# Kernel tuning notes

Hardware: AMD Instinct MI355X
Metric: run time of the kernel (lower is better)

## Reference

```python
import jax, jax.numpy as jnp
import numpy as np

B, CIN, C, H, W = 2, 64, 128, 64, 1024
H2, W2 = H // 2, W // 2

def _unfold(x, k, pad, stride, dil=1):
    # F.unfold equivalent -> [B, C, k*k, Ho, Wo] with (kh, kw) row-major ordering
    Bx, Cx, Hx, Wx = x.shape
    Ho = (Hx + 2 * pad - dil * (k - 1) - 1) // stride + 1
    Wo = (Wx + 2 * pad - dil * (k - 1) - 1) // stride + 1
    xp = jnp.pad(x, ((0, 0), (0, 0), (pad, pad), (pad, pad)))
    pats = [xp[:, :, i * dil:i * dil + stride * (Ho - 1) + 1:stride,
                  j * dil:j * dil + stride * (Wo - 1) + 1:stride]
            for i in range(k) for j in range(k)]
    return jnp.stack(pats, axis=2)

def _conv(x, w, b, pad, dil=1):
    y = jax.lax.conv_general_dilated(x, w, (1, 1), ((pad, pad), (pad, pad)),
                                     rhs_dilation=(dil, dil),
                                     dimension_numbers=('NCHW', 'OIHW', 'NCHW'))
    return y + b[None, :, None, None]

def _c1x1(x, w, b):
    return jnp.einsum('oi,bi...->bo...', w, x) + b.reshape((1, -1) + (1,) * (x.ndim - 2))

def _bn(x, s, b):
    shp = (1, -1) + (1,) * (x.ndim - 2)
    return x * s.reshape(shp) + b.reshape(shp)

def _forward(x, xyz, c1_w, c1_b, c2_w, c2_b, c3_w, c3_b, c4_w, c4_b, c5_w, c5_b,
             rbn_s, rbn_b, p_w, p_b, pbn_s, pbn_b, lin_w, lin_b,
             w1_w, w1_b, w2_w, w2_b, w3_w, w3_b,
             wbn1_s, wbn1_b, wbn2_s, wbn2_b, wbn3_s, wbn3_b):
    lrelu, relu = jax.nn.leaky_relu, jax.nn.relu
    # get_group_mask geometry (kernel 5, stride 2): relative neighbor coordinates
    gxyz = _unfold(xyz, 5, 2, 2) - xyz[:, :, ::2, ::2][:, :, None]  # [B,3,25,H2,W2]
    # ResBlock trunk (eval-mode BN folded to per-channel scale/shift)
    shortcut = lrelu(_c1x1(x, c1_w, c1_b))
    resA1 = _bn(lrelu(_conv(x, c2_w, c2_b, pad=1)), rbn_s[0], rbn_b[0])
    resA2 = _bn(lrelu(_conv(resA1, c3_w, c3_b, pad=2, dil=2)), rbn_s[1], rbn_b[1])
    resA3 = _bn(lrelu(_conv(resA2, c4_w, c4_b, pad=1, dil=2)), rbn_s[2], rbn_b[2])
    concat = jnp.concatenate([resA1, resA2, resA3], axis=1)
    resA = _bn(lrelu(_c1x1(concat, c5_w, c5_b)), rbn_s[3], rbn_b[3]) + shortcut
    # PConv downsample: pointwise MLP, WeightNet on geometry, unfold + per-pixel matmul
    h = resA
    for i in range(3):
        h = relu(_bn(_c1x1(h, p_w[i], p_b[i]), pbn_s[i], pbn_b[i]))
    wn = relu(_bn(_c1x1(gxyz, w1_w, w1_b), wbn1_s, wbn1_b))
    wn = relu(_bn(_c1x1(wn, w2_w, w2_b), wbn2_s, wbn2_b))
    wn = relu(_bn(_c1x1(wn, w3_w, w3_b), wbn3_s, wbn3_b))          # [B,16,25,H2,W2]
    unf = _unfold(h, 5, 2, 2)                                      # [B,C,25,H2,W2]
    y = jnp.einsum('bckhw,bnkhw->bcnhw', unf, wn).reshape(B, C * 16, H2, W2)
    resB = relu(_bn(_c1x1(y, lin_w, lin_b), pbn_s[3], pbn_b[3]))   # [B,C,H2,W2]
    return resB, resA

def setup_inputs():
    keys = iter(jax.random.split(jax.random.key(0), 48))
    def rn(shape, scale=0.05):
        return jax.random.normal(next(keys), shape, jnp.float32) * scale
    def bn_pair(shape):
        return 1.0 + rn(shape, 0.1), rn(shape, 0.1)
    d = {}
    d['x'] = rn((B, CIN, H, W), 1.0)
    d['xyz'] = rn((B, 3, H, W), 0.1)
    d['c1_w'], d['c1_b'] = rn((C, CIN)), rn((C,))
    d['c2_w'], d['c2_b'] = rn((C, CIN, 3, 3)), rn((C,))
    d['c3_w'], d['c3_b'] = rn((C, C, 3, 3)), rn((C,))
    d['c4_w'], d['c4_b'] = rn((C, C, 2, 2)), rn((C,))
    d['c5_w'], d['c5_b'] = rn((C, 3 * C)), rn((C,))
    d['rbn_s'], d['rbn_b'] = bn_pair((4, C))
    d['p_w'], d['p_b'] = rn((3, C, C)), rn((3, C))
    d['pbn_s'], d['pbn_b'] = bn_pair((4, C))
    d['lin_w'], d['lin_b'] = rn((C, 16 * C), 0.02), rn((C,))
    d['w1_w'], d['w1_b'] = rn((8, 3), 0.5), rn((8,))
    d['w2_w'], d['w2_b'] = rn((8, 8), 0.5), rn((8,))
    d['w3_w'], d['w3_b'] = rn((16, 8), 0.5), rn((16,))
    d['wbn1_s'], d['wbn1_b'] = bn_pair((8,))
    d['wbn2_s'], d['wbn2_b'] = bn_pair((8,))
    d['wbn3_s'], d['wbn3_b'] = bn_pair((16,))
    return d

def reference(x, xyz, c1_w, c1_b, c2_w, c2_b, c3_w, c3_b, c4_w, c4_b, c5_w, c5_b,
              rbn_s, rbn_b, p_w, p_b, pbn_s, pbn_b, lin_w, lin_b,
              w1_w, w1_b, w2_w, w2_b, w3_w, w3_b,
              wbn1_s, wbn1_b, wbn2_s, wbn2_b, wbn3_s, wbn3_b):
    return _forward(x, xyz, c1_w, c1_b, c2_w, c2_b, c3_w, c3_b, c4_w, c4_b, c5_w, c5_b,
                    rbn_s, rbn_b, p_w, p_b, pbn_s, pbn_b, lin_w, lin_b,
                    w1_w, w1_b, w2_w, w2_b, w3_w, w3_b,
                    wbn1_s, wbn1_b, wbn2_s, wbn2_b, wbn3_s, wbn3_b)
```

## Files before the change

### kernel.cpp

```cpp
#include <hip/hip_runtime.h>
#include <hip/hip_bf16.h>

typedef __hip_bfloat16 bf16;
typedef unsigned short u16;
typedef unsigned int   u32;

#define B_   2
#define CIN_ 64
#define C_   128
#define H_   64
#define W_   1024
#define HW_  (H_*W_)
#define H2_  32
#define W2_  512
#define HW2_ (H2_*W2_)

typedef __attribute__((ext_vector_type(8))) short bf16x8;
typedef __attribute__((ext_vector_type(4))) float f32x4;

#define OFF_C2  0
#define OFF_C3  73728
#define OFF_C4  221184
#define OFF_C5  286720
#define OFF_C1  335872
#define OFF_PW  344064
#define OFF_LIN 393216
#define WTS_TOT 655360
__device__ __align__(16) u16 g_wts[WTS_TOT];
__device__ __align__(16) u16 g_b1[(size_t)B_*C_*HW_];
__device__ __align__(16) u16 g_b2[(size_t)B_*C_*HW_];
__device__ __align__(16) u16 g_b3[(size_t)B_*C_*HW_];
__device__ __align__(16) u16 g_xb[(size_t)B_*HW_*CIN_];

__device__ __forceinline__ float bits2f(u16 u){
    u32 x = ((u32)u) << 16; float f; __builtin_memcpy(&f, &x, 4); return f;
}
__device__ __forceinline__ u16 f2bits(float v){
    bf16 h = __float2bfloat16(v); u16 u; __builtin_memcpy(&u, &h, 2); return u;
}
__device__ __forceinline__ float lrelu(float v){ return v > 0.f ? v : 0.01f*v; }
__device__ __forceinline__ float relu (float v){ return v > 0.f ? v : 0.f; }

#define LSTR 40
#define PSTR 136
#define TSTR 136

__device__ __forceinline__ void stage_A(u16* As, const u16* w, int wstr, int col0, int tid)
{
#pragma unroll
    for (int r = 0; r < 2; r++) {
        int e = tid + 256*r;
        int co = e >> 2, ch = e & 3;
        *(uint4*)&As[co*LSTR + ch*8] = *(const uint4*)&w[co*wstr + col0 + ch*8];
    }
}

__device__ __forceinline__ void stage_B_pm(u16* Bs, const u16* src, int rowStride,
                                           int kc, int tid)
{
#pragma unroll
    for (int r = 0; r < 2; r++) {
        int e = tid + 256*r;
        int j = e >> 2, g = e & 3;
        *(uint4*)&Bs[j*LSTR + g*8] =
            *(const uint4*)&src[(size_t)j*rowStride + kc*32 + g*8];
    }
}

__device__ __forceinline__ void mfma_step_s(const u16* As, const u16* Bs, int bstr, int koff,
                                            int lane, int wm, int wn_, f32x4 acc[4][4])
{
    const int quad = lane >> 4, l15 = lane & 15;
    bf16x8 a[4], b[4];
#pragma unroll
    for (int i = 0; i < 4; i++)
        a[i] = *(const bf16x8*)&As[(wm*64 + i*16 + l15)*LSTR + quad*8];
#pragma unroll
    for (int j = 0; j < 4; j++)
        b[j] = *(const bf16x8*)&Bs[(wn_*64 + j*16 + l15)*bstr + koff + quad*8];
#pragma unroll
    for (int i = 0; i < 4; i++)
#pragma unroll
        for (int j = 0; j < 4; j++)
            acc[i][j] = __builtin_amdgcn_mfma_f32_16x16x32_bf16(a[i], b[j], acc[i][j], 0, 0, 0);
}

__device__ __forceinline__ void mfma_step(const u16* As, const u16* Bs,
                                          int lane, int wm, int wn_, f32x4 acc[4][4])
{
    mfma_step_s(As, Bs, LSTR, 0, lane, wm, wn_, acc);
}

__device__ __forceinline__ void init_bias(f32x4 acc[4][4], const float* bias, int wm, int lane)
{
    const int quad = lane >> 4;
#pragma unroll
    for (int i = 0; i < 4; i++)
#pragma unroll
        for (int r = 0; r < 4; r++) {
            float bv = bias[wm*64 + i*16 + quad*4 + r];
#pragma unroll
            for (int j = 0; j < 4; j++) acc[i][j][r] = bv;
        }
}

#define XTS 70
__global__ __launch_bounds__(256)
void k_xtrans(const float* __restrict__ x0, u16* __restrict__ xb0)
{
    __shared__ __align__(16) u16 T[128*XTS];
    const int tid = threadIdx.x;
    const float* x = x0 + (size_t)blockIdx.y*CIN_*HW_;
    u16* xb = xb0 + (size_t)blockIdx.y*HW_*CIN_;
    const int pix0 = blockIdx.x * 128;
#pragma unroll
    for (int r = 0; r < 8; r++) {
        int e = tid + 256*r;
        int c = e >> 5, p4 = (e & 31)*4;
        float4 v = *(const float4*)&x[(size_t)c*HW_ + pix0 + p4];
        T[(p4+0)*XTS + c] = f2bits(v.x);
        T[(p4+1)*XTS + c] = f2bits(v.y);
        T[(p4+2)*XTS + c] = f2bits(v.z);
        T[(p4+3)*XTS + c] = f2bits(v.w);
    }
    __syncthreads();
#pragma unroll
    for (int r = 0; r < 4; r++) {
        int e = tid + 256*r;
        int p = e >> 3, g = e & 7;
        const u16* s = &T[p*XTS + g*8];
        u16* d = &xb[(size_t)(pix0+p)*CIN_ + g*8];
        *(uint2*)&d[0] = *(const uint2*)&s[0];
        *(uint2*)&d[4] = *(const uint2*)&s[4];
    }
}

template<int CI, int KS, int DIL, int PAD>
__global__ __launch_bounds__(256)
void k_conv(const u16* __restrict__ in0, const u16* __restrict__ wT,
            const float* __restrict__ bias, const float* __restrict__ bns,
            const float* __restrict__ bnb, u16* __restrict__ out0)
{
    __shared__ __align__(16) u16 S[128*TSTR];
    u16* As = S;
    u16* Bs = S + 128*LSTR;
    const int tid = threadIdx.x, lane = tid & 63, wave = tid >> 6;
    const int wm = wave & 1, wn_ = wave >> 1;
    const u16* in = in0 + (size_t)blockIdx.y*HW_*CI;
    u16* out = out0 + (size_t)blockIdx.y*HW_*C_;
    const int pix0 = blockIdx.x * 128;
    const int y = pix0 >> 10, x0 = pix0 & 1023;

    f32x4 acc[4][4];
    init_bias(acc, bias, wm, lane);

    for (int p = 0; p < KS*KS; p++) {
        int dy = (p/KS)*DIL - PAD, dx = (p%KS)*DIL - PAD;
        int yy = y + dy;
        if (yy < 0 || yy >= H_) continue;
        const u16* srow = in + (size_t)yy*W_*CI;
        for (int kc = 0; kc < CI/32; kc++) {
            stage_A(As, wT + p*128*CI, CI, kc*32, tid);
#pragma unroll
            for (int r = 0; r < 2; r++) {
                int e = tid + 256*r;
                int j = e >> 2, g = e & 3;
                int xx = x0 + dx + j;
                uint4 v = make_uint4(0u, 0u, 0u, 0u);
                if ((unsigned)xx < (unsigned)W_)
                    v = *(const uint4*)&srow[(size_t)xx*CI + kc*32 + g*8];
                *(uint4*)&Bs[j*LSTR + g*8] = v;
            }
            __syncthreads();
            mfma_step(As, Bs, lane, wm, wn_, acc);
            __syncthreads();
        }
    }
    const int quad = lane >> 4, l15 = lane & 15;
    u16* T = S;
#pragma unroll
    for (int i = 0; i < 4; i++)
#pragma unroll
        for (int r = 0; r < 4; r++) {
            int co = wm*64 + i*16 + quad*4 + r;
            float ss = bns[co], tt = bnb[co];
#pragma unroll
            for (int j = 0; j < 4; j++) {
                float v = lrelu(acc[i][j][r]) * ss + tt;
                T[(wn_*64 + j*16 + l15)*TSTR + co] = f2bits(v);
            }
        }
    __syncthreads();
#pragma unroll
    for (int r = 0; r < 8; r++) {
        int e = tid + 256*r;
        int px = e >> 4, g = e & 15;
        *(uint4*)&out[(size_t)(pix0+px)*C_ + g*8] = *(const uint4*)&T[px*TSTR + g*8];
    }
}

__global__ __launch_bounds__(256)
void k_resA(const u16* __restrict__ xb0, const u16* __restrict__ a10,
            const u16* __restrict__ a20, const u16* __restrict__ a30,
            const u16* __restrict__ wc1, const float* __restrict__ c1b,
            const u16* __restrict__ wc5, const float* __restrict__ c5b,
            const float* __restrict__ s3, const float* __restrict__ b3,
            float* __restrict__ out0)
{
    __shared__ __align__(16) u16 As[128*LSTR];
    __shared__ __align__(16) u16 Bs[128*LSTR];
    const int tid = threadIdx.x, lane = tid & 63, wave = tid >> 6;
    const int wm = wave & 1, wn_ = wave >> 1;
    const int b = blockIdx.y;
    const u16* xb = xb0 + (size_t)b*HW_*CIN_;
    const u16* aa[3] = { a10 + (size_t)b*HW_*C_, a20 + (size_t)b*HW_*C_, a30 + (size_t)b*HW_*C_ };
    float* out = out0 + (size_t)b*C_*HW_;
    const int pix0 = blockIdx.x * 128;
    const int quad = lane >> 4, l15 = lane & 15;

    f32x4 acc[4][4];
    init_bias(acc, c1b, wm, lane);
    for (int kc = 0; kc < 2; kc++) {
        stage_A(As, wc1, 64, kc*32, tid);
        stage_B_pm(Bs, xb + (size_t)pix0*CIN_, CIN_, kc, tid);
        __syncthreads();
        mfma_step(As, Bs, lane, wm, wn_, acc);
        __syncthreads();
    }
    float sc[4][4][4];
#pragma unroll
    for (int i = 0; i < 4; i++)
#pragma unroll
        for (int j = 0; j < 4; j++)
#pragma unroll
            for (int r = 0; r < 4; r++) sc[i][j][r] = lrelu(acc[i][j][r]);

    init_bias(acc, c5b, wm, lane);
    for (int s = 0; s < 3; s++) {
        const u16* src = aa[s] + (size_t)pix0*C_;
        for (int kc = 0; kc < 4; kc++) {
            stage_A(As, wc5, 384, s*128 + kc*32, tid);
            stage_B_pm(Bs, src, C_, kc, tid);
            __syncthreads();
            mfma_step(As, Bs, lane, wm, wn_, acc);
            __syncthreads();
        }
    }
#pragma unroll
    for (int i = 0; i < 4; i++)
#pragma unroll
        for (int r = 0; r < 4; r++) {
            int co = wm*64 + i*16 + quad*4 + r;
            float ss = s3[co], tt = b3[co];
#pragma unroll
            for (int j = 0; j < 4; j++) {
                float v = lrelu(acc[i][j][r]) * ss + tt + sc[i][j][r];
                out[co*HW_ + pix0 + wn_*64 + j*16 + l15] = v;
            }
        }
}

__global__ __launch_bounds__(256)
void k_pw3(const float* __restrict__ in0, const u16* __restrict__ w,
           const float* __restrict__ pb, const float* __restrict__ ps,
           const float* __restrict__ pbb, u16* __restrict__ out0)
{
    __shared__ __align__(16) u16 As[128*LSTR];
    __shared__ __align__(16) u16 B0[128*PSTR];
    __shared__ __align__(16) u16 B1[128*PSTR];
    const int tid = threadIdx.x, lane = tid & 63, wave = tid >> 6;
    const int wm = wave & 1, wn_ = wave >> 1;
    const int b = blockIdx.y;
    const float* in = in0 + (size_t)b*C_*HW_;
    u16* out = out0 + (size_t)b*C_*HW_;
    const int pix0 = blockIdx.x * 128;
    const int quad = lane >> 4, l15 = lane & 15;

    for (int e = tid; e < 128*32; e += 256) {
        int kk = e >> 5, j4 = (e & 31)*4;
        float4 v = *(const float4*)&in[kk*HW_ + pix0 + j4];
        u16* d = &B0[j4*PSTR + kk];
        d[0]      = f2bits(v.x);
        d[PSTR]   = f2bits(v.y);
        d[2*PSTR] = f2bits(v.z);
        d[3*PSTR] = f2bits(v.w);
    }

    u16* Bc = B0;
    u16* Bn = B1;
#pragma unroll
    for (int L = 0; L < 3; L++) {
        f32x4 acc[4][4];
        init_bias(acc, pb + L*128, wm, lane);
        for (int kc = 0; kc < 4; kc++) {
            stage_A(As, w + L*16384, 128, kc*32, tid);
            __syncthreads();
            mfma_step_s(As, Bc, PSTR, kc*32, lane, wm, wn_, acc);
            __syncthreads();
        }
        const float* ss = ps + L*128;
        const float* tt = pbb + L*128;
        if (L < 2) {
#pragma unroll
            for (int i = 0; i < 4; i++)
#pragma unroll
                for (int r = 0; r < 4; r++) {
                    int co = wm*64 + i*16 + quad*4 + r;
                    float s1 = ss[co], t1 = tt[co];
#pragma unroll
                    for (int j = 0; j < 4; j++) {
                        float v = relu(acc[i][j][r] * s1 + t1);
                        Bn[(wn_*64 + j*16 + l15)*PSTR + co] = f2bits(v);
                    }
                }
            u16* t = Bc; Bc = Bn; Bn = t;
        } else {
#pragma unroll
            for (int i = 0; i < 4; i++)
#pragma unroll
                for (int r = 0; r < 4; r++) {
                    int co = wm*64 + i*16 + quad*4 + r;
                    float s1 = ss[co], t1 = tt[co];
#pragma unroll
                    for (int j = 0; j < 4; j++) {
                        float v = relu(acc[i][j][r] * s1 + t1);
                        out[co*HW_ + pix0 + wn_*64 + j*16 + l15] = f2bits(v);
                    }
                }
        }
    }
}

__global__ __launch_bounds__(256)
void wn_kernel(const float* __restrict__ xyz0,
               const float* __restrict__ w1w, const float* __restrict__ w1b,
               const float* __restrict__ w2w, const float* __restrict__ w2b,
               const float* __restrict__ w3w, const float* __restrict__ w3b,
               const float* __restrict__ s1, const float* __restrict__ bb1,
               const float* __restrict__ s2, const float* __restrict__ bb2,
               const float* __restrict__ s3, const float* __restrict__ bb3,
               u16* __restrict__ out0)
{
    const float* xyz = xyz0 + (size_t)blockIdx.y*3*HW_;
    u16* out = out0 + (size_t)blockIdx.y*400*HW2_;
    int idx = blockIdx.x*256 + threadIdx.x;
    int j = idx & (W2_-1); int t = idx >> 9;
    int i = t & (H2_-1);   int k = t >> 5;
    int kh = k / 5, kw = k - kh*5;
    int yy = 2*i + kh - 2, xx = 2*j + kw - 2;
    bool inr = (yy >= 0 && yy < H_ && xx >= 0 && xx < W_);

    float g[3];
#pragma unroll
    for (int c = 0; c < 3; c++) {
        float ctr = xyz[c*HW_ + (2*i)*W_ + 2*j];
        float v = inr ? xyz[c*HW_ + yy*W_ + xx] : 0.f;
        g[c] = v - ctr;
    }
    float a1[8];
#pragma unroll
    for (int n = 0; n < 8; n++) {
        float v = w1b[n];
#pragma unroll
        for (int c = 0; c < 3; c++) v += w1w[n*3 + c] * g[c];
        a1[n] = relu(v * s1[n] + bb1[n]);
    }
    float a2[8];
#pragma unroll
    for (int n = 0; n < 8; n++) {
        float v = w2b[n];
#pragma unroll
        for (int m = 0; m < 8; m++) v += w2w[n*8 + m] * a1[m];
        a2[n] = relu(v * s2[n] + bb2[n]);
    }
#pragma unroll
    for (int n = 0; n < 16; n++) {
        float v = w3b[n];
#pragma unroll
        for (int m = 0; m < 8; m++) v += w3w[n*8 + m] * a2[m];
        v = relu(v * s3[n] + bb3[n]);
        out[(n*25 + k)*HW2_ + i*W2_ + j] = f2bits(v);
    }
}

__global__ __launch_bounds__(512)
void k_yfused(const u16* __restrict__ h0, const u16* __restrict__ wn0,
              const u16* __restrict__ w, const float* __restrict__ bias,
              const float* __restrict__ bns, const float* __restrict__ bnb,
              float* __restrict__ out0)
{
    __shared__ __align__(16) float slab[40*148];
    __shared__ __align__(16) u16 Bs[64*PSTR];
    const int tid = threadIdx.x;
    const int bx = blockIdx.x;
    const int j0 = (bx & 7) * 64;
    const int i2 = bx >> 3;
    const int b  = blockIdx.y;
    const u16* h  = h0  + (size_t)b*C_*HW_;
    const u16* wn = wn0 + (size_t)b*400*HW2_;
    float* out = out0 + (size_t)b*C_*HW2_;

    const int n = tid & 15, pxq = tid >> 4;
    const int lane = tid & 63, wave = tid >> 6;
    const int wm4 = wave & 3, wnp = wave >> 2;
    const int quad = lane >> 4, l15 = lane & 15;

    float wnreg[25][2];
    {
        const u16* wb = wn + (n*25)*HW2_ + i2*W2_ + j0 + pxq*2;
#pragma unroll
        for (int k = 0; k < 25; k++) {
            u32 t = *(const u32*)(wb + k*HW2_);
            wnreg[k][0] = bits2f((u16)(t & 0xffff));
            wnreg[k][1] = bits2f((u16)(t >> 16));
        }
    }

    const int bA0 = (wm4*32 +  0 + l15)*2048 + quad*8;
    const int bA1 = (wm4*32 + 16 + l15)*2048 + quad*8;

    f32x4 acc[2][2];
#pragma unroll
    for (int i = 0; i < 2; i++)
#pragma unroll
        for (int r = 0; r < 4; r++) {
            float bv = bias[wm4*32 + i*16 + quad*4 + r];
            acc[i][0][r] = bv;
            acc[i][1][r] = bv;
        }

    for (int c0 = 0; c0 < 128; c0 += 8) {
        __syncthreads();
        for (int e = tid; e < 720; e += 512) {
            int cc = e / 90, rem = e - cc*90;
            int rr = rem / 18, g = rem - rr*18;
            int yy = 2*i2 + rr - 2;
            int xs0 = 2*j0 - 8 + 8*g;
            float f[8];
            if ((unsigned)yy < (unsigned)H_ && (unsigned)xs0 <= (unsigned)(W_-8)) {
                uint4 v = *(const uint4*)&h[(c0+cc)*HW_ + yy*W_ + xs0];
                f[0] = bits2f((u16)(v.x & 0xffff)); f[1] = bits2f((u16)(v.x >> 16));
                f[2] = bits2f((u16)(v.y & 0xffff)); f[3] = bits2f((u16)(v.y >> 16));
                f[4] = bits2f((u16)(v.z & 0xffff)); f[5] = bits2f((u16)(v.z >> 16));
                f[6] = bits2f((u16)(v.w & 0xffff)); f[7] = bits2f((u16)(v.w >> 16));
            } else if ((unsigned)yy < (unsigned)H_) {
#pragma unroll
                for (int m = 0; m < 8; m++) {
                    int xs = xs0 + m;
                    f[m] = ((unsigned)xs < (unsigned)W_)
                         ? bits2f(h[(c0+cc)*HW_ + yy*W_ + xs]) : 0.f;
                }
            } else {
#pragma unroll
                for (int m = 0; m < 8; m++) f[m] = 0.f;
            }
            float* d = &slab[(cc*5 + rr)*148 + 2 + 8*g];
            *(float2*)(d+0) = make_float2(f[0], f[1]);
            *(float2*)(d+2) = make_float2(f[2], f[3]);
            *(float2*)(d+4) = make_float2(f[4], f[5]);
            *(float2*)(d+6) = make_float2(f[6], f[7]);
        }
        bf16x8 af0[4], af1[4];
#pragma unroll
        for (int kc = 0; kc < 4; kc++) {
            af0[kc] = *(const bf16x8*)&w[bA0 + c0*16 + kc*32];
            af1[kc] = *(const bf16x8*)&w[bA1 + c0*16 + kc*32];
        }
        __syncthreads();
#pragma unroll 2
        for (int cc = 0; cc < 8; cc++) {
            float yv0 = 0.f, yv1 = 0.f;
#pragma unroll
            for (int rr = 0; rr < 5; rr++) {
                const float* fr = &slab[(cc*5 + rr)*148 + 8 + 4*pxq];
                float4 A  = *(const float4*)fr;
                float4 Bv = *(const float4*)(fr + 4);
                yv0 += A.x*wnreg[rr*5+0][0] + A.y*wnreg[rr*5+1][0]
                     + A.z*wnreg[rr*5+2][0] + A.w*wnreg[rr*5+3][0]
                     + Bv.x*wnreg[rr*5+4][0];
                yv1 += A.z*wnreg[rr*5+0][1] + A.w*wnreg[rr*5+1][1]
                     + Bv.x*wnreg[rr*5+2][1] + Bv.y*wnreg[rr*5+3][1]
                     + Bv.z*wnreg[rr*5+4][1];
            }
            Bs[(2*pxq)  *PSTR + cc*16 + n] = f2bits(yv0);
            Bs[(2*pxq+1)*PSTR + cc*16 + n] = f2bits(yv1);
        }
        __syncthreads();
#pragma unroll
        for (int kc = 0; kc < 4; kc++) {
            bf16x8 b0 = *(const bf16x8*)&Bs[(wnp*32 +  0 + l15)*PSTR + kc*32 + quad*8];
            bf16x8 b1 = *(const bf16x8*)&Bs[(wnp*32 + 16 + l15)*PSTR + kc*32 + quad*8];
            acc[0][0] = __builtin_amdgcn_mfma_f32_16x16x32_bf16(af0[kc], b0, acc[0][0], 0, 0, 0);
            acc[0][1] = __builtin_amdgcn_mfma_f32_16x16x32_bf16(af0[kc], b1, acc[0][1], 0, 0, 0);
            acc[1][0] = __builtin_amdgcn_mfma_f32_16x16x32_bf16(af1[kc], b0, acc[1][0], 0, 0, 0);
            acc[1][1] = __builtin_amdgcn_mfma_f32_16x16x32_bf16(af1[kc], b1, acc[1][1], 0, 0, 0);
        }
    }
#pragma unroll
    for (int i = 0; i < 2; i++)
#pragma unroll
        for (int r = 0; r < 4; r++) {
            int co = wm4*32 + i*16 + quad*4 + r;
            float ss = bns[co], tt = bnb[co];
#pragma unroll
            for (int j = 0; j < 2; j++) {
                float v = relu(acc[i][j][r] * ss + tt);
                out[co*HW2_ + i2*W2_ + j0 + wnp*32 + j*16 + l15] = v;
            }
        }
}

__global__ __launch_bounds__(256)
void k_wtrans(const float* __restrict__ c2w, const float* __restrict__ c3w,
              const float* __restrict__ c4w, const float* __restrict__ c5w,
              const float* __restrict__ c1w, const float* __restrict__ pw,
              const float* __restrict__ linw)
{
    int i = blockIdx.x*256 + threadIdx.x;
    if (i >= WTS_TOT) return;
    float v;
    if (i < OFF_C3) {
        int p = i / 8192, rem = i - p*8192;
        int co = rem >> 6, ci = rem & 63;
        v = c2w[(co*64 + ci)*9 + p];
    } else if (i < OFF_C4) {
        int t = i - OFF_C3;
        int p = t / 16384, rem = t - p*16384;
        int co = rem >> 7, ci = rem & 127;
        v = c3w[(co*128 + ci)*9 + p];
    } else if (i < OFF_C5) {
        int t = i - OFF_C4;
        int p = t / 16384, rem = t - p*16384;
        int co = rem >> 7, ci = rem & 127;
        v = c4w[(co*128 + ci)*4 + p];
    } else if (i < OFF_C1)  v = c5w[i - OFF_C5];
    else if (i < OFF_PW)    v = c1w[i - OFF_C1];
    else if (i < OFF_LIN)   v = pw[i - OFF_PW];
    else                    v = linw[i - OFF_LIN];
    g_wts[i] = f2bits(v);
}

extern "C" void kernel_launch(void* const* d_in, const int* in_sizes, int n_in,
                              void* d_out, int out_size, void* d_ws, size_t ws_size,
                              hipStream_t stream)
{
    const float* x     = (const float*)d_in[0];
    const float* xyz   = (const float*)d_in[1];
    const float* c1_w  = (const float*)d_in[2];
    const float* c1_b  = (const float*)d_in[3];
    const float* c2_w  = (const float*)d_in[4];
    const float* c2_b  = (const float*)d_in[5];
    const float* c3_w  = (const float*)d_in[6];
    const float* c3_b  = (const float*)d_in[7];
    const float* c4_w  = (const float*)d_in[8];
    const float* c4_b  = (const float*)d_in[9];
    const float* c5_w  = (const float*)d_in[10];
    const float* c5_b  = (const float*)d_in[11];
    const float* rbn_s = (const float*)d_in[12];
    const float* rbn_b = (const float*)d_in[13];
    const float* p_w   = (const float*)d_in[14];
    const float* p_b   = (const float*)d_in[15];
    const float* pbn_s = (const float*)d_in[16];
    const float* pbn_b = (const float*)d_in[17];
    const float* lin_w = (const float*)d_in[18];
    const float* lin_b = (const float*)d_in[19];
    const float* w1_w  = (const float*)d_in[20];
    const float* w1_b  = (const float*)d_in[21];
    const float* w2_w  = (const float*)d_in[22];
    const float* w2_b  = (const float*)d_in[23];
    const float* w3_w  = (const float*)d_in[24];
    const float* w3_b  = (const float*)d_in[25];
    const float* wbn1_s = (const float*)d_in[26];
    const float* wbn1_b = (const float*)d_in[27];
    const float* wbn2_s = (const float*)d_in[28];
    const float* wbn2_b = (const float*)d_in[29];
    const float* wbn3_s = (const float*)d_in[30];
    const float* wbn3_b = (const float*)d_in[31];

    float* outB = (float*)d_out;
    float* outA = outB + (size_t)B_*C_*HW2_;

    u16 *wts, *b1, *b2, *b3, *xb;
    { void* p; hipGetSymbolAddress(&p, HIP_SYMBOL(g_wts)); wts = (u16*)p; }
    { void* p; hipGetSymbolAddress(&p, HIP_SYMBOL(g_b1));  b1  = (u16*)p; }
    { void* p; hipGetSymbolAddress(&p, HIP_SYMBOL(g_b2));  b2  = (u16*)p; }
    { void* p; hipGetSymbolAddress(&p, HIP_SYMBOL(g_b3));  b3  = (u16*)p; }
    { void* p; hipGetSymbolAddress(&p, HIP_SYMBOL(g_xb));  xb  = (u16*)p; }

    dim3 blk(256);

    k_wtrans<<<dim3((WTS_TOT + 255)/256), blk, 0, stream>>>(c2_w, c3_w, c4_w, c5_w,
                                                            c1_w, p_w, lin_w);
    k_xtrans<<<dim3(512, B_), blk, 0, stream>>>(x, xb);
    k_conv<64,3,1,1><<<dim3(512, B_), blk, 0, stream>>>(xb, wts+OFF_C2, c2_b,
                                                        rbn_s, rbn_b, b1);
    k_conv<128,3,2,2><<<dim3(512, B_), blk, 0, stream>>>(b1, wts+OFF_C3, c3_b,
                                                         rbn_s+128, rbn_b+128, b2);
    k_conv<128,2,2,1><<<dim3(512, B_), blk, 0, stream>>>(b2, wts+OFF_C4, c4_b,
                                                         rbn_s+256, rbn_b+256, b3);
    k_resA<<<dim3(512, B_), blk, 0, stream>>>(xb, b1, b2, b3, wts+OFF_C1, c1_b,
                                              wts+OFF_C5, c5_b, rbn_s+384, rbn_b+384, outA);
    k_pw3<<<dim3(512, B_), blk, 0, stream>>>(outA, wts+OFF_PW, p_b, pbn_s, pbn_b, b1);
    wn_kernel<<<dim3(1600, B_), blk, 0, stream>>>(xyz, w1_w, w1_b, w2_w, w2_b, w3_w, w3_b,
                                                  wbn1_s, wbn1_b, wbn2_s, wbn2_b,
                                                  wbn3_s, wbn3_b, b2);
    k_yfused<<<dim3(256, B_), dim3(512), 0, stream>>>(b1, b2, wts+OFF_LIN, lin_b,
                                                      pbn_s+384, pbn_b+384, outB);
}
```

Measured before the change: 571.6 us.

## Load weight fragments directly from global memory and stage full-K input tiles once

Weight (A) tiles are no longer copied into shared memory. MFMA A-fragments are read directly from global or L2 cached weights, and the whole input channel depth for each tap or segment is staged into LDS in one pass. This removes per-32-K staging and roughly halves the __syncthreads barriers in the conv, resA and pw3 kernels. In exchange, every wave re-reads weights from global memory with strided 16-byte loads, which increases L2 traffic and can expose load latency without LDS reuse.

```diff
diff --git a/kernel.cpp b/kernel.cpp
--- a/kernel.cpp
+++ b/kernel.cpp
@@ -41,54 +41,26 @@
 __device__ __forceinline__ float lrelu(float v){ return v > 0.f ? v : 0.01f*v; }
 __device__ __forceinline__ float relu (float v){ return v > 0.f ? v : 0.f; }
 
-#define LSTR 40
 #define PSTR 136
 #define TSTR 136
 
-__device__ __forceinline__ void stage_A(u16* As, const u16* w, int wstr, int col0, int tid)
-{
-#pragma unroll
-    for (int r = 0; r < 2; r++) {
-        int e = tid + 256*r;
-        int co = e >> 2, ch = e & 3;
-        *(uint4*)&As[co*LSTR + ch*8] = *(const uint4*)&w[co*wstr + col0 + ch*8];
-    }
-}
-
-__device__ __forceinline__ void stage_B_pm(u16* Bs, const u16* src, int rowStride,
-                                           int kc, int tid)
-{
-#pragma unroll
-    for (int r = 0; r < 2; r++) {
-        int e = tid + 256*r;
-        int j = e >> 2, g = e & 3;
-        *(uint4*)&Bs[j*LSTR + g*8] =
-            *(const uint4*)&src[(size_t)j*rowStride + kc*32 + g*8];
-    }
-}
-
-__device__ __forceinline__ void mfma_step_s(const u16* As, const u16* Bs, int bstr, int koff,
-                                            int lane, int wm, int wn_, f32x4 acc[4][4])
+__device__ __forceinline__ void mfma_k32(const u16* __restrict__ wA, int wstr, int aoff,
+                                         const u16* Bs, int bstr, int boff,
+                                         int lane, int wm, int wn_, f32x4 acc[4][4])
 {
     const int quad = lane >> 4, l15 = lane & 15;
     bf16x8 a[4], b[4];
 #pragma unroll
     for (int i = 0; i < 4; i++)
-        a[i] = *(const bf16x8*)&As[(wm*64 + i*16 + l15)*LSTR + quad*8];
+        a[i] = *(const bf16x8*)&wA[(size_t)(wm*64 + i*16 + l15)*wstr + aoff + quad*8];
 #pragma unroll
     for (int j = 0; j < 4; j++)
-        b[j] = *(const bf16x8*)&Bs[(wn_*64 + j*16 + l15)*bstr + koff + quad*8];
+        b[j] = *(const bf16x8*)&Bs[(wn_*64 + j*16 + l15)*bstr + boff + quad*8];
 #pragma unroll
     for (int i = 0; i < 4; i++)
 #pragma unroll
         for (int j = 0; j < 4; j++)
             acc[i][j] = __builtin_amdgcn_mfma_f32_16x16x32_bf16(a[i], b[j], acc[i][j], 0, 0, 0);
-}
-
-__device__ __forceinline__ void mfma_step(const u16* As, const u16* Bs,
-                                          int lane, int wm, int wn_, f32x4 acc[4][4])
-{
-    mfma_step_s(As, Bs, LSTR, 0, lane, wm, wn_, acc);
 }
 
 __device__ __forceinline__ void init_bias(f32x4 acc[4][4], const float* bias, int wm, int lane)
@@ -141,9 +113,7 @@
             const float* __restrict__ bias, const float* __restrict__ bns,
             const float* __restrict__ bnb, u16* __restrict__ out0)
 {
-    __shared__ __align__(16) u16 S[128*TSTR];
-    u16* As = S;
-    u16* Bs = S + 128*LSTR;
+    __shared__ __align__(16) u16 Bs[128*PSTR];
     const int tid = threadIdx.x, lane = tid & 63, wave = tid >> 6;
     const int wm = wave & 1, wn_ = wave >> 1;
     const u16* in = in0 + (size_t)blockIdx.y*HW_*CI;
@@ -159,25 +129,39 @@
         int yy = y + dy;
         if (yy < 0 || yy >= H_) continue;
         const u16* srow = in + (size_t)yy*W_*CI;
-        for (int kc = 0; kc < CI/32; kc++) {
-            stage_A(As, wT + p*128*CI, CI, kc*32, tid);
-#pragma unroll
-            for (int r = 0; r < 2; r++) {
+        const u16* wp = wT + p*128*CI;
+        __syncthreads();
+        if (CI == 128) {
+#pragma unroll
+            for (int r = 0; r < 8; r++) {
                 int e = tid + 256*r;
-                int j = e >> 2, g = e & 3;
-                int xx = x0 + dx + j;
+                int px = e >> 4, g = e & 15;
+                int xx = x0 + dx + px;
                 uint4 v = make_uint4(0u, 0u, 0u, 0u);
                 if ((unsigned)xx < (unsigned)W_)
-                    v = *(const uint4*)&srow[(size_t)xx*CI + kc*32 + g*8];
-                *(uint4*)&Bs[j*LSTR + g*8] = v;
-            }
-            __syncthreads();
-            mfma_step(As, Bs, lane, wm, wn_, acc);
-            __syncthreads();
-        }
+                    v = *(const uint4*)&srow[(size_t)xx*CI + g*8];
+                *(uint4*)&Bs[px*PSTR + g*8] = v;
+            }
+        } else {
+#pragma unroll
+            for (int r = 0; r < 4; r++) {
+                int e = tid + 256*r;
+                int px = e >> 3, g = e & 7;
+                int xx = x0 + dx + px;
+                uint4 v = make_uint4(0u, 0u, 0u, 0u);
+                if ((unsigned)xx < (unsigned)W_)
+                    v = *(const uint4*)&srow[(size_t)xx*CI + g*8];
+                *(uint4*)&Bs[px*PSTR + g*8] = v;
+            }
+        }
+        __syncthreads();
+#pragma unroll
+        for (int kc = 0; kc < CI/32; kc++)
+            mfma_k32(wp, CI, kc*32, Bs, PSTR, kc*32, lane, wm, wn_, acc);
     }
     const int quad = lane >> 4, l15 = lane & 15;
-    u16* T = S;
+    u16* T = Bs;
+    __syncthreads();
 #pragma unroll
     for (int i = 0; i < 4; i++)
 #pragma unroll
@@ -207,8 +191,7 @@
             const float* __restrict__ s3, const float* __restrict__ b3,
             float* __restrict__ out0)
 {
-    __shared__ __align__(16) u16 As[128*LSTR];
-    __shared__ __align__(16) u16 Bs[128*LSTR];
+    __shared__ __align__(16) u16 Bs[128*PSTR];
     const int tid = threadIdx.x, lane = tid & 63, wave = tid >> 6;
     const int wm = wave & 1, wn_ = wave >> 1;
     const int b = blockIdx.y;
@@ -220,13 +203,17 @@
 
     f32x4 acc[4][4];
     init_bias(acc, c1b, wm, lane);
-    for (int kc = 0; kc < 2; kc++) {
-        stage_A(As, wc1, 64, kc*32, tid);
-        stage_B_pm(Bs, xb + (size_t)pix0*CIN_, CIN_, kc, tid);
-        __syncthreads();
-        mfma_step(As, Bs, lane, wm, wn_, acc);
-        __syncthreads();
-    }
+#pragma unroll
+    for (int r = 0; r < 4; r++) {
+        int e = tid + 256*r;
+        int px = e >> 3, g = e & 7;
+        *(uint4*)&Bs[px*PSTR + g*8] = *(const uint4*)&xb[(size_t)(pix0+px)*CIN_ + g*8];
+    }
+    __syncthreads();
+#pragma unroll
+    for (int kc = 0; kc < 2; kc++)
+        mfma_k32(wc1, 64, kc*32, Bs, PSTR, kc*32, lane, wm, wn_, acc);
+
     float sc[4][4][4];
 #pragma unroll
     for (int i = 0; i < 4; i++)
@@ -238,13 +225,17 @@
     init_bias(acc, c5b, wm, lane);
     for (int s = 0; s < 3; s++) {
         const u16* src = aa[s] + (size_t)pix0*C_;
-        for (int kc = 0; kc < 4; kc++) {
-            stage_A(As, wc5, 384, s*128 + kc*32, tid);
-            stage_B_pm(Bs, src, C_, kc, tid);
-            __syncthreads();
-            mfma_step(As, Bs, lane, wm, wn_, acc);
-            __syncthreads();
-        }
+        __syncthreads();
+#pragma unroll
+        for (int r = 0; r < 8; r++) {
+            int e = tid + 256*r;
+            int px = e >> 4, g = e & 15;
+            *(uint4*)&Bs[px*PSTR + g*8] = *(const uint4*)&src[(size_t)px*C_ + g*8];
+        }
+        __syncthreads();
+#pragma unroll
+        for (int kc = 0; kc < 4; kc++)
+            mfma_k32(wc5, 384, s*128 + kc*32, Bs, PSTR, kc*32, lane, wm, wn_, acc);
     }
 #pragma unroll
     for (int i = 0; i < 4; i++)
@@ -265,7 +256,6 @@
            const float* __restrict__ pb, const float* __restrict__ ps,
            const float* __restrict__ pbb, u16* __restrict__ out0)
 {
-    __shared__ __align__(16) u16 As[128*LSTR];
     __shared__ __align__(16) u16 B0[128*PSTR];
     __shared__ __align__(16) u16 B1[128*PSTR];
     const int tid = threadIdx.x, lane = tid & 63, wave = tid >> 6;
@@ -292,12 +282,10 @@
     for (int L = 0; L < 3; L++) {
         f32x4 acc[4][4];
         init_bias(acc, pb + L*128, wm, lane);
-        for (int kc = 0; kc < 4; kc++) {
-            stage_A(As, w + L*16384, 128, kc*32, tid);
-            __syncthreads();
-            mfma_step_s(As, Bc, PSTR, kc*32, lane, wm, wn_, acc);
-            __syncthreads();
-        }
+        __syncthreads();
+#pragma unroll
+        for (int kc = 0; kc < 4; kc++)
+            mfma_k32(w + L*16384, 128, kc*32, Bc, PSTR, kc*32, lane, wm, wn_, acc);
         const float* ss = ps + L*128;
         const float* tt = pbb + L*128;
         if (L < 2) {
```

Result: slower. 680.2 us (+19.0%).

## Reuse staged input row window across horizontal taps in dilated conv kernel

Applied to the files above, without the earlier changes.

The conv kernel now stages, per kernel row and channel chunk, one widened input window (136 pixels) and all KS weight taps for that row into shared memory. It then runs the KS horizontal taps by shifting the B-operand read offset, instead of restaging input and weights for every tap. This removes repeated global loads and cuts the number of barrier pairs per tap. In exchange it uses more LDS per block, which may lower occupancy, and it adds a fixed window width that must cover PAD and DIL.

```diff
diff --git a/kernel.cpp b/kernel.cpp
--- a/kernel.cpp
+++ b/kernel.cpp
@@ -141,11 +141,15 @@
             const float* __restrict__ bias, const float* __restrict__ bns,
             const float* __restrict__ bnb, u16* __restrict__ out0)
 {
-    __shared__ __align__(16) u16 S[128*TSTR];
+    constexpr int WTOT = 136;
+    constexpr int ASZ  = KS*128*LSTR;
+    constexpr int SSZ  = (ASZ + WTOT*LSTR) > 128*TSTR ? (ASZ + WTOT*LSTR) : 128*TSTR;
+    __shared__ __align__(16) u16 S[SSZ];
     u16* As = S;
-    u16* Bs = S + 128*LSTR;
+    u16* Bs = S + ASZ;
     const int tid = threadIdx.x, lane = tid & 63, wave = tid >> 6;
     const int wm = wave & 1, wn_ = wave >> 1;
+    const int quad = lane >> 4, l15 = lane & 15;
     const u16* in = in0 + (size_t)blockIdx.y*HW_*CI;
     u16* out = out0 + (size_t)blockIdx.y*HW_*C_;
     const int pix0 = blockIdx.x * 128;
@@ -154,30 +158,46 @@
     f32x4 acc[4][4];
     init_bias(acc, bias, wm, lane);
 
-    for (int p = 0; p < KS*KS; p++) {
-        int dy = (p/KS)*DIL - PAD, dx = (p%KS)*DIL - PAD;
-        int yy = y + dy;
+    for (int dyi = 0; dyi < KS; dyi++) {
+        int yy = y + dyi*DIL - PAD;
         if (yy < 0 || yy >= H_) continue;
         const u16* srow = in + (size_t)yy*W_*CI;
         for (int kc = 0; kc < CI/32; kc++) {
-            stage_A(As, wT + p*128*CI, CI, kc*32, tid);
-#pragma unroll
-            for (int r = 0; r < 2; r++) {
-                int e = tid + 256*r;
-                int j = e >> 2, g = e & 3;
-                int xx = x0 + dx + j;
+            __syncthreads();
+            for (int e = tid; e < KS*512; e += 256) {
+                int d = e >> 9, rem = e & 511;
+                int co = rem >> 2, ch = rem & 3;
+                *(uint4*)&As[d*128*LSTR + co*LSTR + ch*8] =
+                    *(const uint4*)&wT[(size_t)(dyi*KS + d)*128*CI + co*CI + kc*32 + ch*8];
+            }
+            for (int e = tid; e < WTOT*4; e += 256) {
+                int wpx = e >> 2, g = e & 3;
+                int xx = x0 - PAD + wpx;
                 uint4 v = make_uint4(0u, 0u, 0u, 0u);
                 if ((unsigned)xx < (unsigned)W_)
                     v = *(const uint4*)&srow[(size_t)xx*CI + kc*32 + g*8];
-                *(uint4*)&Bs[j*LSTR + g*8] = v;
+                *(uint4*)&Bs[wpx*LSTR + g*8] = v;
             }
             __syncthreads();
-            mfma_step(As, Bs, lane, wm, wn_, acc);
-            __syncthreads();
-        }
-    }
-    const int quad = lane >> 4, l15 = lane & 15;
+#pragma unroll
+            for (int d = 0; d < KS; d++) {
+                bf16x8 a[4], bb[4];
+#pragma unroll
+                for (int i = 0; i < 4; i++)
+                    a[i] = *(const bf16x8*)&As[d*128*LSTR + (wm*64 + i*16 + l15)*LSTR + quad*8];
+#pragma unroll
+                for (int j = 0; j < 4; j++)
+                    bb[j] = *(const bf16x8*)&Bs[(wn_*64 + j*16 + l15 + d*DIL)*LSTR + quad*8];
+#pragma unroll
+                for (int i = 0; i < 4; i++)
+#pragma unroll
+                    for (int j = 0; j < 4; j++)
+                        acc[i][j] = __builtin_amdgcn_mfma_f32_16x16x32_bf16(a[i], bb[j], acc[i][j], 0, 0, 0);
+            }
+        }
+    }
     u16* T = S;
+    __syncthreads();
 #pragma unroll
     for (int i = 0; i < 4; i++)
 #pragma unroll
```

New measurement: 570.0 us. Within noise of the previous version (-0.3%).
